# Kernel tuning notes

Hardware: AMD Instinct MI355X
Metric: run time of the kernel (lower is better)

The kernel has to match this reference:

```python
import jax, jax.numpy as jnp
import numpy as np

NUM_CLASSES = 512  # static number of distinct labels (all present in targets)
EPS = 1e-8         # torch.nn.CosineSimilarity default eps


def setup_inputs() -> dict:
    N, D, C = 65536, 256, NUM_CLASSES
    key = jax.random.key(0)
    k1, k2 = jax.random.split(key)
    inputs = jax.random.normal(k1, (N, D), dtype=jnp.float32)
    # every label 0..C-1 appears -> sorted-unique remap in the torch code is identity
    targets = jax.random.permutation(k2, jnp.arange(N, dtype=jnp.int32) % C)
    return {"inputs": inputs, "targets": targets}


def reference(inputs, targets):
    C = NUM_CLASSES
    # per-label segment mean (prototypes), replacing the python unique/mask loop
    sums = jax.ops.segment_sum(inputs, targets, num_segments=C)          # [C, D]
    counts = jax.ops.segment_sum(jnp.ones((inputs.shape[0],), inputs.dtype),
                                 targets, num_segments=C)                # [C]
    protos = sums / counts[:, None]                                       # [C, D]

    # pairwise cosine similarity: x.p / max(|x||p|, eps)
    dots = inputs @ protos.T                                              # [N, C]
    n_in = jnp.linalg.norm(inputs, axis=-1)                               # [N]
    n_pr = jnp.linalg.norm(protos, axis=-1)                               # [C]
    sim = dots / jnp.maximum(n_in[:, None] * n_pr[None, :], EPS)          # [N, C]

    # cross entropy, mean reduction (labels already equal mapped targets)
    logp = jax.nn.log_softmax(sim, axis=-1)                               # [N, C]
    nll = -jnp.take_along_axis(logp, targets[:, None].astype(jnp.int32), axis=-1)[:, 0]
    return jnp.mean(nll)
```

## Files before the change

### kernel.cpp

```cpp
#include <hip/hip_runtime.h>
#include <hip/hip_bf16.h>
#include <math.h>

#define NROWS 65536
#define DIM   256
#define NCLS  512
#define CPW   128
#define NSUB  2
#define BMAIN (64 * NSUB)
#define NBLK  (NROWS / BMAIN)

#define WS_CNT_I   0
#define WS_IDX_I   512
#define WS_QPACK_F 66048

typedef float f32x4  __attribute__((ext_vector_type(4)));
typedef short bf16x8 __attribute__((ext_vector_type(8)));
typedef unsigned short u16;

__device__ inline u16 f2bf(float f) {
  unsigned u = __float_as_uint(f);
  u += 0x7FFFu + ((u >> 16) & 1u);
  return (u16)(u >> 16);
}
__device__ inline unsigned pack2(float a, float b) {
  __hip_bfloat162 h = __float22bfloat162_rn(make_float2(a, b));
  return *reinterpret_cast<unsigned*>(&h);
}

#define DPP_ADD(x, ctrl)                                                   \
  (x) += __int_as_float(__builtin_amdgcn_update_dpp(                       \
      __float_as_int(x), __float_as_int(x), (ctrl), 0xF, 0xF, false))
__device__ inline float dpp_sum8(float x) {
  DPP_ADD(x, 0xB1); DPP_ADD(x, 0x4E); DPP_ADD(x, 0x141); return x;
}
__device__ inline float dpp_sum16(float x) {
  DPP_ADD(x, 0xB1); DPP_ADD(x, 0x4E); DPP_ADD(x, 0x141); DPP_ADD(x, 0x140);
  return x;
}

__global__ __launch_bounds__(512) void k_zero(int* __restrict__ cnt,
                                              float* __restrict__ out) {
  cnt[threadIdx.x] = 0;
  if (threadIdx.x == 0) out[0] = 0.f;
}

__global__ __launch_bounds__(256) void k_scatter(
    const int* __restrict__ tgt, int* __restrict__ cnt, int* __restrict__ idx) {
  const int row = blockIdx.x * 256 + threadIdx.x;
  const int c = tgt[row];
  const int p = atomicAdd(&cnt[c], 1);
  if (p < CPW) idx[c * CPW + p] = row;
}

__global__ __launch_bounds__(512) void k_csum(
    const float* __restrict__ x, const int* __restrict__ idx,
    u16* __restrict__ qpack) {
  __shared__ int   sidx[CPW];
  __shared__ float wpart[8][DIM];
  __shared__ float wsum[4];
  __shared__ float ninv_s;
  const int c    = blockIdx.x;
  const int tid  = threadIdx.x;
  const int w    = tid >> 6;
  const int lane = tid & 63;
  if (tid < CPW) sidx[tid] = idx[c * CPW + tid];
  __syncthreads();

  float4 v[16];
  #pragma unroll
  for (int j = 0; j < 16; ++j) {
    const int row = sidx[w * 16 + j];
    v[j] = *reinterpret_cast<const float4*>(x + (size_t)row * DIM + lane * 4);
  }
  #pragma unroll
  for (int st = 8; st >= 1; st >>= 1) {
    #pragma unroll
    for (int j = 0; j < st; ++j) {
      v[j].x += v[j + st].x; v[j].y += v[j + st].y;
      v[j].z += v[j + st].z; v[j].w += v[j + st].w;
    }
  }
  *reinterpret_cast<float4*>(&wpart[w][lane * 4]) = v[0];
  __syncthreads();

  float s = 0.f;
  if (tid < DIM) {
    #pragma unroll
    for (int ww = 0; ww < 8; ++ww) s += wpart[ww][tid];
  }
  float sq = dpp_sum16(s * s);
  sq += __shfl_xor(sq, 16, 64);
  sq += __shfl_xor(sq, 32, 64);
  if (tid < DIM && (tid & 63) == 0) wsum[tid >> 6] = sq;
  __syncthreads();
  if (tid == 0) ninv_s = rsqrtf(fmaxf(wsum[0] + wsum[1] + wsum[2] + wsum[3], 1e-30f));
  __syncthreads();
  if (tid < DIM)
    qpack[((tid >> 3) * NCLS + c) * 8 + (tid & 7)] = f2bf(s * ninv_s);
}

__device__ inline void normpack(const float4 v[8], u16* __restrict__ dst,
                                int row, int part) {
  float ss = 0.f;
  #pragma unroll
  for (int j = 0; j < 8; ++j)
    ss += v[j].x * v[j].x + v[j].y * v[j].y + v[j].z * v[j].z + v[j].w * v[j].w;
  ss = dpp_sum8(ss);
  const float rn = rsqrtf(fmaxf(ss, 1e-30f));
  #pragma unroll
  for (int jj = 0; jj < 4; ++jj) {
    uint4 wv;
    wv.x = pack2(v[2*jj].x * rn,   v[2*jj].y * rn);
    wv.y = pack2(v[2*jj].z * rn,   v[2*jj].w * rn);
    wv.z = pack2(v[2*jj+1].x * rn, v[2*jj+1].y * rn);
    wv.w = pack2(v[2*jj+1].z * rn, v[2*jj+1].w * rn);
    const int kg = part * 4 + jj;
    const int rs = row ^ part;
    *reinterpret_cast<uint4*>(&dst[(kg * 64 + rs) * 8]) = wv;
  }
}

__global__ __launch_bounds__(512, 4) void k_main(
    const float* __restrict__ x, const int* __restrict__ tgt,
    const u16* __restrict__ qpack, float* __restrict__ out) {
  __shared__ u16   Alds[NSUB][32 * 64 * 8] __attribute__((aligned(16)));
  __shared__ float psum[8][64];
  __shared__ float simt[64];
  __shared__ int   ltgt[BMAIN];

  const int tid  = threadIdx.x;
  const int w    = tid >> 6;
  const int lane = tid & 63;
  const int lg   = lane >> 4, l15 = lane & 15;
  const int row  = tid >> 3;
  const int part = tid & 7;
  const size_t rbase = (size_t)blockIdx.x * BMAIN;

  const bf16x8* bp = reinterpret_cast<const bf16x8*>(qpack);
  const int bbase = w * 64 + l15;

  float4 v[8];
  {
    const float4* xr = reinterpret_cast<const float4*>(
        x + (rbase + row) * DIM + part * 32);
    #pragma unroll
    for (int j = 0; j < 8; ++j) v[j] = xr[j];
  }
  if (tid < BMAIN) ltgt[tid] = tgt[rbase + tid];
  normpack(v, &Alds[0][0], row, part);
  __syncthreads();

  float block_loss = 0.f;

  #pragma unroll
  for (int s = 0; s < NSUB; ++s) {
    if (s + 1 < NSUB) {
      const float4* xr = reinterpret_cast<const float4*>(
          x + (rbase + (s + 1) * 64 + row) * DIM + part * 32);
      #pragma unroll
      for (int j = 0; j < 8; ++j) v[j] = xr[j];
    }

    f32x4 acc[4][4];
    #pragma unroll
    for (int m = 0; m < 4; ++m)
      #pragma unroll
      for (int n = 0; n < 4; ++n) acc[m][n] = (f32x4)0.f;

    const u16* al = &Alds[s][0];

    bf16x8 B0[4], B1[4];
    #pragma unroll
    for (int n = 0; n < 4; ++n) B0[n] = bp[lg * NCLS + bbase + n * 16];

    #pragma unroll 1
    for (int kk = 0; kk < 8; kk += 2) {
      #pragma unroll
      for (int n = 0; n < 4; ++n)
        B1[n] = bp[((kk + 1) * 4 + lg) * NCLS + bbase + n * 16];
      {
        const int arow = (lg + kk * 4) * 64;
        bf16x8 a[4];
        #pragma unroll
        for (int m = 0; m < 4; ++m)
          a[m] = *reinterpret_cast<const bf16x8*>(
              &al[(arow + ((m * 16 + l15) ^ kk)) * 8]);
        #pragma unroll
        for (int m = 0; m < 4; ++m)
          #pragma unroll
          for (int n = 0; n < 4; ++n)
            acc[m][n] = __builtin_amdgcn_mfma_f32_16x16x32_bf16(a[m], B0[n], acc[m][n], 0, 0, 0);
      }
      const int k2 = (kk + 2) & 7;
      #pragma unroll
      for (int n = 0; n < 4; ++n)
        B0[n] = bp[(k2 * 4 + lg) * NCLS + bbase + n * 16];
      {
        const int arow = (lg + (kk + 1) * 4) * 64;
        bf16x8 a[4];
        #pragma unroll
        for (int m = 0; m < 4; ++m)
          a[m] = *reinterpret_cast<const bf16x8*>(
              &al[(arow + ((m * 16 + l15) ^ (kk + 1))) * 8]);
        #pragma unroll
        for (int m = 0; m < 4; ++m)
          #pragma unroll
          for (int n = 0; n < 4; ++n)
            acc[m][n] = __builtin_amdgcn_mfma_f32_16x16x32_bf16(a[m], B1[n], acc[m][n], 0, 0, 0);
      }
    }

    #pragma unroll
    for (int m = 0; m < 4; ++m) {
      #pragma unroll
      for (int reg = 0; reg < 4; ++reg) {
        const int r = m * 16 + lg * 4 + reg;
        float sx = __expf(acc[m][0][reg]) + __expf(acc[m][1][reg]) +
                   __expf(acc[m][2][reg]) + __expf(acc[m][3][reg]);
        sx = dpp_sum16(sx);
        if (l15 == 0) psum[w][r] = sx;
        const int tg = ltgt[s * 64 + r];
        if (w == (tg >> 6) && l15 == (tg & 15)) {
          const int nt = (tg >> 4) & 3;
          float pv = acc[m][0][reg];
          pv = (nt == 1) ? acc[m][1][reg] : pv;
          pv = (nt == 2) ? acc[m][2][reg] : pv;
          pv = (nt == 3) ? acc[m][3][reg] : pv;
          simt[r] = pv;
        }
      }
    }
    __syncthreads();
    if (tid < 64) {
      float sum = 0.f;
      #pragma unroll
      for (int ww = 0; ww < 8; ++ww) sum += psum[ww][tid];
      float lr = __logf(sum) - simt[tid];
      lr = dpp_sum16(lr);
      lr += __shfl_xor(lr, 16, 64);
      lr += __shfl_xor(lr, 32, 64);
      block_loss += lr;
    }
    if (s + 1 < NSUB) {
      normpack(v, &Alds[s + 1][0], row, part);
      __syncthreads();
    }
  }
  if (tid == 0) atomicAdd(out, block_loss * (1.0f / (float)NROWS));
}

extern "C" void kernel_launch(void* const* d_in, const int* in_sizes, int n_in,
                              void* d_out, int out_size, void* d_ws, size_t ws_size,
                              hipStream_t stream) {
  const float* x   = (const float*)d_in[0];
  const int*   tgt = (const int*)d_in[1];
  float* ws    = (float*)d_ws;
  int*   cnt   = (int*)ws + WS_CNT_I;
  int*   idx   = (int*)ws + WS_IDX_I;
  u16*   qpack = (u16*)(ws + WS_QPACK_F);
  float* out   = (float*)d_out;

  k_zero<<<1, 512, 0, stream>>>(cnt, out);
  k_scatter<<<NROWS / 256, 256, 0, stream>>>(tgt, cnt, idx);
  k_csum<<<NCLS, 512, 0, stream>>>(x, idx, qpack);
  k_main<<<NBLK, 512, 0, stream>>>(x, tgt, qpack, out);
}
```

Before: 77.30 us.

## Split class-sum into partial blocks, add qnorm kernel, shrink main tile

The per-class prototype sum is split across four blocks per class that write partial sums, and a new kernel reduces them, normalizes, packs to bf16 and zeroes the output. The main kernel drops its two-subtile software pipeline and processes 64 rows per block, doubling the grid. The zero kernel is replaced with hipMemsetAsync. The intent is more parallelism in the prototype stage and more blocks in the main stage, at the cost of an extra launch, a workspace round trip for partial sums, and twice as many atomics on the output.

```diff
diff --git a/kernel.cpp b/kernel.cpp
--- a/kernel.cpp
+++ b/kernel.cpp
@@ -6,13 +6,13 @@
 #define DIM   256
 #define NCLS  512
 #define CPW   128
-#define NSUB  2
-#define BMAIN (64 * NSUB)
-#define NBLK  (NROWS / BMAIN)
+#define BM    64
+#define NBLK  (NROWS / BM)
 
 #define WS_CNT_I   0
 #define WS_IDX_I   512
 #define WS_QPACK_F 66048
+#define WS_QPART_F 131584
 
 typedef float f32x4  __attribute__((ext_vector_type(4)));
 typedef short bf16x8 __attribute__((ext_vector_type(8)));
@@ -37,12 +37,6 @@
 __device__ inline float dpp_sum16(float x) {
   DPP_ADD(x, 0xB1); DPP_ADD(x, 0x4E); DPP_ADD(x, 0x141); DPP_ADD(x, 0x140);
   return x;
-}
-
-__global__ __launch_bounds__(512) void k_zero(int* __restrict__ cnt,
-                                              float* __restrict__ out) {
-  cnt[threadIdx.x] = 0;
-  if (threadIdx.x == 0) out[0] = 0.f;
 }
 
 __global__ __launch_bounds__(256) void k_scatter(
@@ -53,28 +47,28 @@
   if (p < CPW) idx[c * CPW + p] = row;
 }
 
-__global__ __launch_bounds__(512) void k_csum(
+__global__ __launch_bounds__(256) void k_csum_part(
     const float* __restrict__ x, const int* __restrict__ idx,
-    u16* __restrict__ qpack) {
-  __shared__ int   sidx[CPW];
-  __shared__ float wpart[8][DIM];
-  __shared__ float wsum[4];
-  __shared__ float ninv_s;
-  const int c    = blockIdx.x;
+    float* __restrict__ qpart) {
+  __shared__ int   sidx[32];
+  __shared__ float wpart[4][DIM];
+  const int b    = blockIdx.x;
+  const int c    = b >> 2;
+  const int q    = b & 3;
   const int tid  = threadIdx.x;
   const int w    = tid >> 6;
   const int lane = tid & 63;
-  if (tid < CPW) sidx[tid] = idx[c * CPW + tid];
-  __syncthreads();
-
-  float4 v[16];
-  #pragma unroll
-  for (int j = 0; j < 16; ++j) {
-    const int row = sidx[w * 16 + j];
+  if (tid < 32) sidx[tid] = idx[c * CPW + q * 32 + tid];
+  __syncthreads();
+
+  float4 v[8];
+  #pragma unroll
+  for (int j = 0; j < 8; ++j) {
+    const int row = sidx[w * 8 + j];
     v[j] = *reinterpret_cast<const float4*>(x + (size_t)row * DIM + lane * 4);
   }
   #pragma unroll
-  for (int st = 8; st >= 1; st >>= 1) {
+  for (int st = 4; st >= 1; st >>= 1) {
     #pragma unroll
     for (int j = 0; j < st; ++j) {
       v[j].x += v[j + st].x; v[j].y += v[j + st].y;
@@ -84,20 +78,29 @@
   *reinterpret_cast<float4*>(&wpart[w][lane * 4]) = v[0];
   __syncthreads();
 
-  float s = 0.f;
-  if (tid < DIM) {
-    #pragma unroll
-    for (int ww = 0; ww < 8; ++ww) s += wpart[ww][tid];
-  }
+  const float s = wpart[0][tid] + wpart[1][tid] + wpart[2][tid] + wpart[3][tid];
+  qpart[(size_t)b * DIM + tid] = s;
+}
+
+__global__ __launch_bounds__(256) void k_qnorm(
+    const float* __restrict__ qpart, u16* __restrict__ qpack,
+    float* __restrict__ out) {
+  __shared__ float wsum[4];
+  __shared__ float ninv_s;
+  const int c = blockIdx.x, d = threadIdx.x;
+  if (c == 0 && d == 0) out[0] = 0.f;
+  float s = qpart[(size_t)(c * 4 + 0) * DIM + d] +
+            qpart[(size_t)(c * 4 + 1) * DIM + d] +
+            qpart[(size_t)(c * 4 + 2) * DIM + d] +
+            qpart[(size_t)(c * 4 + 3) * DIM + d];
   float sq = dpp_sum16(s * s);
   sq += __shfl_xor(sq, 16, 64);
   sq += __shfl_xor(sq, 32, 64);
-  if (tid < DIM && (tid & 63) == 0) wsum[tid >> 6] = sq;
-  __syncthreads();
-  if (tid == 0) ninv_s = rsqrtf(fmaxf(wsum[0] + wsum[1] + wsum[2] + wsum[3], 1e-30f));
-  __syncthreads();
-  if (tid < DIM)
-    qpack[((tid >> 3) * NCLS + c) * 8 + (tid & 7)] = f2bf(s * ninv_s);
+  if ((d & 63) == 0) wsum[d >> 6] = sq;
+  __syncthreads();
+  if (d == 0) ninv_s = rsqrtf(fmaxf(wsum[0] + wsum[1] + wsum[2] + wsum[3], 1e-30f));
+  __syncthreads();
+  qpack[((d >> 3) * NCLS + c) * 8 + (d & 7)] = f2bf(s * ninv_s);
 }
 
 __device__ inline void normpack(const float4 v[8], u16* __restrict__ dst,
@@ -124,10 +127,10 @@
 __global__ __launch_bounds__(512, 4) void k_main(
     const float* __restrict__ x, const int* __restrict__ tgt,
     const u16* __restrict__ qpack, float* __restrict__ out) {
-  __shared__ u16   Alds[NSUB][32 * 64 * 8] __attribute__((aligned(16)));
+  __shared__ u16   Alds[32 * 64 * 8] __attribute__((aligned(16)));
   __shared__ float psum[8][64];
   __shared__ float simt[64];
-  __shared__ int   ltgt[BMAIN];
+  __shared__ int   ltgt[BM];
 
   const int tid  = threadIdx.x;
   const int w    = tid >> 6;
@@ -135,119 +138,101 @@
   const int lg   = lane >> 4, l15 = lane & 15;
   const int row  = tid >> 3;
   const int part = tid & 7;
-  const size_t rbase = (size_t)blockIdx.x * BMAIN;
-
-  const bf16x8* bp = reinterpret_cast<const bf16x8*>(qpack);
-  const int bbase = w * 64 + l15;
-
-  float4 v[8];
+  const size_t rbase = (size_t)blockIdx.x * BM;
+
+  if (tid < BM) ltgt[tid] = tgt[rbase + tid];
+
   {
     const float4* xr = reinterpret_cast<const float4*>(
         x + (rbase + row) * DIM + part * 32);
+    float4 v[8];
     #pragma unroll
     for (int j = 0; j < 8; ++j) v[j] = xr[j];
-  }
-  if (tid < BMAIN) ltgt[tid] = tgt[rbase + tid];
-  normpack(v, &Alds[0][0], row, part);
-  __syncthreads();
-
-  float block_loss = 0.f;
-
-  #pragma unroll
-  for (int s = 0; s < NSUB; ++s) {
-    if (s + 1 < NSUB) {
-      const float4* xr = reinterpret_cast<const float4*>(
-          x + (rbase + (s + 1) * 64 + row) * DIM + part * 32);
-      #pragma unroll
-      for (int j = 0; j < 8; ++j) v[j] = xr[j];
-    }
-
-    f32x4 acc[4][4];
-    #pragma unroll
-    for (int m = 0; m < 4; ++m)
-      #pragma unroll
-      for (int n = 0; n < 4; ++n) acc[m][n] = (f32x4)0.f;
-
-    const u16* al = &Alds[s][0];
-
-    bf16x8 B0[4], B1[4];
-    #pragma unroll
-    for (int n = 0; n < 4; ++n) B0[n] = bp[lg * NCLS + bbase + n * 16];
-
-    #pragma unroll 1
-    for (int kk = 0; kk < 8; kk += 2) {
-      #pragma unroll
-      for (int n = 0; n < 4; ++n)
-        B1[n] = bp[((kk + 1) * 4 + lg) * NCLS + bbase + n * 16];
-      {
-        const int arow = (lg + kk * 4) * 64;
-        bf16x8 a[4];
+    normpack(v, &Alds[0], row, part);
+  }
+  __syncthreads();
+
+  const bf16x8* bp = reinterpret_cast<const bf16x8*>(qpack);
+  const int bbase = w * 64 + l15;
+
+  f32x4 acc[4][4];
+  #pragma unroll
+  for (int m = 0; m < 4; ++m)
+    #pragma unroll
+    for (int n = 0; n < 4; ++n) acc[m][n] = (f32x4)0.f;
+
+  bf16x8 B0[4], B1[4];
+  #pragma unroll
+  for (int n = 0; n < 4; ++n) B0[n] = bp[lg * NCLS + bbase + n * 16];
+
+  #pragma unroll 1
+  for (int kk = 0; kk < 8; kk += 2) {
+    #pragma unroll
+    for (int n = 0; n < 4; ++n)
+      B1[n] = bp[((kk + 1) * 4 + lg) * NCLS + bbase + n * 16];
+    {
+      const int arow = (lg + kk * 4) * 64;
+      bf16x8 a[4];
+      #pragma unroll
+      for (int m = 0; m < 4; ++m)
+        a[m] = *reinterpret_cast<const bf16x8*>(
+            &Alds[(arow + ((m * 16 + l15) ^ kk)) * 8]);
+      #pragma unroll
+      for (int m = 0; m < 4; ++m)
         #pragma unroll
-        for (int m = 0; m < 4; ++m)
-          a[m] = *reinterpret_cast<const bf16x8*>(
-              &al[(arow + ((m * 16 + l15) ^ kk)) * 8]);
+        for (int n = 0; n < 4; ++n)
+          acc[m][n] = __builtin_amdgcn_mfma_f32_16x16x32_bf16(a[m], B0[n], acc[m][n], 0, 0, 0);
+    }
+    const int k2 = (kk + 2) & 7;
+    #pragma unroll
+    for (int n = 0; n < 4; ++n)
+      B0[n] = bp[(k2 * 4 + lg) * NCLS + bbase + n * 16];
+    {
+      const int arow = (lg + (kk + 1) * 4) * 64;
+      bf16x8 a[4];
+      #pragma unroll
+      for (int m = 0; m < 4; ++m)
+        a[m] = *reinterpret_cast<const bf16x8*>(
+            &Alds[(arow + ((m * 16 + l15) ^ (kk + 1))) * 8]);
+      #pragma unroll
+      for (int m = 0; m < 4; ++m)
         #pragma unroll
-        for (int m = 0; m < 4; ++m)
-          #pragma unroll
-          for (int n = 0; n < 4; ++n)
-            acc[m][n] = __builtin_amdgcn_mfma_f32_16x16x32_bf16(a[m], B0[n], acc[m][n], 0, 0, 0);
+        for (int n = 0; n < 4; ++n)
+          acc[m][n] = __builtin_amdgcn_mfma_f32_16x16x32_bf16(a[m], B1[n], acc[m][n], 0, 0, 0);
+    }
+  }
+
+  #pragma unroll
+  for (int m = 0; m < 4; ++m) {
+    #pragma unroll
+    for (int reg = 0; reg < 4; ++reg) {
+      const int r = m * 16 + lg * 4 + reg;
+      float sx = __expf(acc[m][0][reg]) + __expf(acc[m][1][reg]) +
+                 __expf(acc[m][2][reg]) + __expf(acc[m][3][reg]);
+      sx = dpp_sum16(sx);
+      if (l15 == 0) psum[w][r] = sx;
+      const int tg = ltgt[r];
+      if (w == (tg >> 6) && l15 == (tg & 15)) {
+        const int nt = (tg >> 4) & 3;
+        float pv = acc[m][0][reg];
+        pv = (nt == 1) ? acc[m][1][reg] : pv;
+        pv = (nt == 2) ? acc[m][2][reg] : pv;
+        pv = (nt == 3) ? acc[m][3][reg] : pv;
+        simt[r] = pv;
       }
-      const int k2 = (kk + 2) & 7;
-      #pragma unroll
-      for (int n = 0; n < 4; ++n)
-        B0[n] = bp[(k2 * 4 + lg) * NCLS + bbase + n * 16];
-      {
-        const int arow = (lg + (kk + 1) * 4) * 64;
-        bf16x8 a[4];
-        #pragma unroll
-        for (int m = 0; m < 4; ++m)
-          a[m] = *reinterpret_cast<const bf16x8*>(
-              &al[(arow + ((m * 16 + l15) ^ (kk + 1))) * 8]);
-        #pragma unroll
-        for (int m = 0; m < 4; ++m)
-          #pragma unroll
-          for (int n = 0; n < 4; ++n)
-            acc[m][n] = __builtin_amdgcn_mfma_f32_16x16x32_bf16(a[m], B1[n], acc[m][n], 0, 0, 0);
-      }
-    }
-
-    #pragma unroll
-    for (int m = 0; m < 4; ++m) {
-      #pragma unroll
-      for (int reg = 0; reg < 4; ++reg) {
-        const int r = m * 16 + lg * 4 + reg;
-        float sx = __expf(acc[m][0][reg]) + __expf(acc[m][1][reg]) +
-                   __expf(acc[m][2][reg]) + __expf(acc[m][3][reg]);
-        sx = dpp_sum16(sx);
-        if (l15 == 0) psum[w][r] = sx;
-        const int tg = ltgt[s * 64 + r];
-        if (w == (tg >> 6) && l15 == (tg & 15)) {
-          const int nt = (tg >> 4) & 3;
-          float pv = acc[m][0][reg];
-          pv = (nt == 1) ? acc[m][1][reg] : pv;
-          pv = (nt == 2) ? acc[m][2][reg] : pv;
-          pv = (nt == 3) ? acc[m][3][reg] : pv;
-          simt[r] = pv;
-        }
-      }
-    }
-    __syncthreads();
-    if (tid < 64) {
-      float sum = 0.f;
-      #pragma unroll
-      for (int ww = 0; ww < 8; ++ww) sum += psum[ww][tid];
-      float lr = __logf(sum) - simt[tid];
-      lr = dpp_sum16(lr);
-      lr += __shfl_xor(lr, 16, 64);
-      lr += __shfl_xor(lr, 32, 64);
-      block_loss += lr;
-    }
-    if (s + 1 < NSUB) {
-      normpack(v, &Alds[s + 1][0], row, part);
-      __syncthreads();
-    }
-  }
-  if (tid == 0) atomicAdd(out, block_loss * (1.0f / (float)NROWS));
+    }
+  }
+  __syncthreads();
+  if (tid < 64) {
+    float sum = 0.f;
+    #pragma unroll
+    for (int ww = 0; ww < 8; ++ww) sum += psum[ww][tid];
+    float lr = __logf(sum) - simt[tid];
+    lr = dpp_sum16(lr);
+    lr += __shfl_xor(lr, 16, 64);
+    lr += __shfl_xor(lr, 32, 64);
+    if (tid == 0) atomicAdd(out, lr * (1.0f / (float)NROWS));
+  }
 }
 
 extern "C" void kernel_launch(void* const* d_in, const int* in_sizes, int n_in,
@@ -259,10 +244,12 @@
   int*   cnt   = (int*)ws + WS_CNT_I;
   int*   idx   = (int*)ws + WS_IDX_I;
   u16*   qpack = (u16*)(ws + WS_QPACK_F);
+  float* qpart = ws + WS_QPART_F;
   float* out   = (float*)d_out;
 
-  k_zero<<<1, 512, 0, stream>>>(cnt, out);
+  hipMemsetAsync(cnt, 0, NCLS * sizeof(int), stream);
   k_scatter<<<NROWS / 256, 256, 0, stream>>>(tgt, cnt, idx);
-  k_csum<<<NCLS, 512, 0, stream>>>(x, idx, qpack);
+  k_csum_part<<<NCLS * 4, 256, 0, stream>>>(x, idx, qpart);
+  k_qnorm<<<NCLS, 256, 0, stream>>>(qpart, qpack, out);
   k_main<<<NBLK, 512, 0, stream>>>(x, tgt, qpack, out);
 }
```

Result: no change. 78.31 us (+1.3%).
